# Optimization experiments

Measured on AMD Instinct MI355X. Metric: run time of the kernel, lower is better.

The kernel has to match this reference:

```python
import jax, jax.numpy as jnp
import numpy as np

NUM_EXPERTS = 8
TOP_K = 2
LORA_ALPHA = 2.0
LORA_RANK = 16
D_MODEL = 2048
D_HIDDEN = 5632


def setup_inputs() -> dict:
    key = jax.random.key(0)
    ks = jax.random.split(key, 11)
    B, S, D, H, E, R = 2, 1024, D_MODEL, D_HIDDEN, NUM_EXPERTS, LORA_RANK
    sd = 1.0 / np.sqrt(D)
    sh = 1.0 / np.sqrt(H)
    x = jax.random.normal(ks[0], (B, S, D), jnp.float32)
    gate_w = jax.random.normal(ks[1], (E, D), jnp.float32) * sd   # router Linear(D->E), no bias
    w_up = jax.random.normal(ks[2], (H, D), jnp.float32) * sd     # up_proj.weight
    w_gate = jax.random.normal(ks[3], (H, D), jnp.float32) * sd   # gate_proj.weight
    w_down = jax.random.normal(ks[4], (D, H), jnp.float32) * sh   # down_proj.weight
    up_A = jax.random.normal(ks[5], (E, R, D), jnp.float32) * sd
    up_B = jax.random.normal(ks[6], (E, H, R), jnp.float32) * 0.02
    gate_A = jax.random.normal(ks[7], (E, R, D), jnp.float32) * sd
    gate_B = jax.random.normal(ks[8], (E, H, R), jnp.float32) * 0.02
    down_A = jax.random.normal(ks[9], (E, R, H), jnp.float32) * sh
    down_B = jax.random.normal(ks[10], (E, D, R), jnp.float32) * 0.02
    return {"x": x, "gate_w": gate_w, "w_up": w_up, "w_gate": w_gate,
            "w_down": w_down, "up_A": up_A, "up_B": up_B,
            "gate_A": gate_A, "gate_B": gate_B, "down_A": down_A, "down_B": down_B}


def reference(x, gate_w, w_up, w_gate, w_down, up_A, up_B, gate_A, gate_B, down_A, down_B):
    B, S, D = x.shape
    H = w_up.shape[0]
    # router: logits [B,S,E], top-k over experts (last dim)
    gate_logits = jnp.einsum('bsd,ed->bse', x, gate_w)
    topw, sel = jax.lax.top_k(gate_logits, TOP_K)            # [B,S,k]
    # NOTE: source applies softmax over dim=1 (the SEQUENCE axis) -- reproduced faithfully
    topw = jax.nn.softmax(topw.astype(jnp.float32), axis=1).astype(x.dtype)
    xt = x.reshape(-1, D)                                    # [T, D]
    wf = topw.reshape(-1, TOP_K)                             # [T, k]
    sf = sel.reshape(-1, TOP_K)                              # [T, k]
    # shared base projections computed once for all tokens
    base_up = xt @ w_up.T                                    # [T, H]
    base_gate = xt @ w_gate.T                                # [T, H]
    mixed_h = jnp.zeros((xt.shape[0], H), x.dtype)
    lora_down = jnp.zeros_like(xt)
    # loop over fixed small expert count; low-rank LoRA deltas applied without
    # materializing full merged weights (same math by linearity of matmul)
    for e in range(NUM_EXPERTS):
        c = jnp.sum(jnp.where(sf == e, wf, 0.0), axis=1)     # [T] routing weight (0 if not routed)
        lo_up = LORA_ALPHA * ((xt @ up_A[e].T) @ up_B[e].T)
        lo_gate = LORA_ALPHA * ((xt @ gate_A[e].T) @ gate_B[e].T)
        h_e = jax.nn.silu(base_up + lo_up) * (base_gate + lo_gate)  # [T, H]
        ch = c[:, None] * h_e
        mixed_h = mixed_h + ch
        lora_down = lora_down + LORA_ALPHA * ((ch @ down_A[e].T) @ down_B[e].T)
    out = mixed_h @ w_down.T + lora_down                     # base down GEMM done once on mixed hidden
    return out.reshape(B, S, D)
```

## Files before the change

kernel.cpp:

```cpp
#include <hip/hip_runtime.h>
#include <hip/hip_fp16.h>
#include <cmath>

#define TOKENS 2048
#define DMODEL 2048
#define DHID   5632
#define NEXP   8
#define RANK   16
#define LALPHA 2.0f

typedef __attribute__((ext_vector_type(4))) float f32x4;
typedef __attribute__((ext_vector_type(8))) short s16x8;
typedef __attribute__((ext_vector_type(4))) short s16x4;
typedef __attribute__((ext_vector_type(8))) _Float16 f16x8;

__device__ __forceinline__ short f2bf(float f){
  unsigned u = __float_as_uint(f);
  u += 0x7fffu + ((u >> 16) & 1u);
  return (short)(u >> 16);
}
__device__ __forceinline__ short f2h(float f){
  return (short)__half_as_ushort(__float2half(f));
}

struct Src2 { const short* s0; const short* s1; };

__device__ __forceinline__ Src2 mk_src(const short* g, long ld, int tid){
  Src2 st;
  const int L0 = tid,      r0 = L0>>2, c0 = ((L0&3) - (r0>>1)) & 3;
  const int L1 = 256+tid,  r1 = L1>>2, c1 = ((L1&3) - (r1>>1)) & 3;
  st.s0 = g + (long)r0*ld + c0*8;
  st.s1 = g + (long)r1*ld + c1*8;
  return st;
}
__device__ __forceinline__ void stage2(const Src2& st, int k0, short* t, int tid){
  __builtin_amdgcn_global_load_lds((const __attribute__((address_space(1))) void*)(st.s0 + k0),
                                   (__attribute__((address_space(3))) void*)(t + tid*8), 16, 0, 0);
  __builtin_amdgcn_global_load_lds((const __attribute__((address_space(1))) void*)(st.s1 + k0),
                                   (__attribute__((address_space(3))) void*)(t + (256+tid)*8), 16, 0, 0);
}
__device__ __forceinline__ s16x8 fragb(const short* t, int row, int quad){
  const int p = (quad + (row>>1)) & 3;
  return *(const s16x8*)(t + (row*4 + p)*8);
}
__device__ __forceinline__ f16x8 fragh(const short* t, int row, int quad){
  const int p = (quad + (row>>1)) & 3;
  return *(const f16x8*)(t + (row*4 + p)*8);
}

struct Stage64 { const short* g; short* t; int off[4]; int dof; };

__device__ __forceinline__ Stage64 mk_stage64(const short* g, long ld, short* t, int tid){
  Stage64 st; st.g = g; st.t = t;
  #pragma unroll
  for(int p=0;p<4;p++){
    const int L = p*256 + tid;
    const int r = L>>3, cp = L&7;
    const int c = (cp - (r&7)) & 7;
    st.off[p] = r*(int)ld + c*8;
  }
  st.dof = tid*8;
  return st;
}
__device__ __forceinline__ void do_stage64(const Stage64& st, int k0){
  #pragma unroll
  for(int p=0;p<4;p++)
    __builtin_amdgcn_global_load_lds(
      (const __attribute__((address_space(1))) void*)(st.g + st.off[p] + k0),
      (__attribute__((address_space(3))) void*)(st.t + st.dof + p*2048), 16, 0, 0);
}
__device__ __forceinline__ s16x8 fragb64(const short* t, int row, int ksub, int quad){
  const int c = ksub*4 + quad;
  const int p = (c + (row&7)) & 7;
  return *(const s16x8*)(t + (row*8 + p)*8);
}
__device__ __forceinline__ f16x8 fragh64(const short* t, int row, int ksub, int quad){
  const int c = ksub*4 + quad;
  const int p = (c + (row&7)) & 7;
  return *(const f16x8*)(t + (row*8 + p)*8);
}

__global__ void k_cast(const float* __restrict__ x, const float* __restrict__ w_up,
                       const float* __restrict__ w_gate, const float* __restrict__ w_down,
                       const float* __restrict__ upA, const float* __restrict__ gateA,
                       const float* __restrict__ downA, const float* __restrict__ upB,
                       const float* __restrict__ gateB, const float* __restrict__ downB,
                       short* __restrict__ xb, short* __restrict__ wub, short* __restrict__ wgb,
                       short* __restrict__ wdb, short* __restrict__ daA, short* __restrict__ acat,
                       short* __restrict__ upBcat, short* __restrict__ gateBcat, short* __restrict__ wdbcat){
  const long e0 = 4194304, e1 = 15728640, e2 = 27262976, e3 = 38797312;
  const long e4 = 39518208, e5 = 40042496, e6 = 40763392, e7 = 41484288, e8 = 41746432;
  const long i = ((long)blockIdx.x*256 + threadIdx.x) * 4;
  if(i >= e8) return;
  const float* src; short* dst; long l; int fp16 = 0;
  if(i < e0){ src = x; dst = xb; l = i; }
  else if(i < e1){ src = w_up; dst = wub; l = i - e0; }
  else if(i < e2){ src = w_gate; dst = wgb; l = i - e1; }
  else if(i < e3){ src = w_down; dst = wdb; l = i - e2; }
  else if(i < e4){ src = downA; dst = daA; l = i - e3; }
  else if(i < e5){
    l = i - e4;
    const long c = l>>11;
    const long e = c>>5, pj = (c>>4)&1, r = c&15;
    src = (pj ? gateA : upA) + ((e*RANK + r)<<11) + (l&2047) - l;
    dst = acat;
  }
  else if(i < e6){
    l = i - e5;
    const long h = l>>7, c = l&127, e = c>>4, r = c&15;
    src = upB + ((e*DHID + h)*RANK + r) - l;
    dst = upBcat; fp16 = 1;
  }
  else if(i < e7){
    l = i - e6;
    const long h = l>>7, c = l&127, e = c>>4, r = c&15;
    src = gateB + ((e*DHID + h)*RANK + r) - l;
    dst = gateBcat; fp16 = 1;
  }
  else {
    l = i - e7;
    const long d = l>>7, c = l&127, e = c>>4, r = c&15;
    src = downB + ((e*DMODEL + d)*RANK + r) - l;
    dst = wdbcat; fp16 = 1;
  }
  const float4 v = *(const float4*)(src + l);
  s16x4 o;
  if(fp16){ o[0]=f2h(v.x); o[1]=f2h(v.y); o[2]=f2h(v.z); o[3]=f2h(v.w); }
  else    { o[0]=f2bf(v.x); o[1]=f2bf(v.y); o[2]=f2bf(v.z); o[3]=f2bf(v.w); }
  *(s16x4*)(dst + l) = o;
}

__global__ void k_router(const float* __restrict__ x, const float* __restrict__ gw,
                         int* __restrict__ sel, float* __restrict__ topv){
  const int t = blockIdx.x*4 + (threadIdx.x>>6);
  const int lane = threadIdx.x & 63;
  const float* xr = x + (long)t * DMODEL;
  float acc[NEXP];
  #pragma unroll
  for(int e=0;e<NEXP;e++) acc[e]=0.f;
  #pragma unroll
  for(int it=0; it<8; it++){
    const int d = it*256 + lane*4;
    const float4 xv = *(const float4*)(xr + d);
    #pragma unroll
    for(int e=0;e<NEXP;e++){
      const float4 wv = *(const float4*)(gw + e*DMODEL + d);
      acc[e] += xv.x*wv.x + xv.y*wv.y + xv.z*wv.z + xv.w*wv.w;
    }
  }
  #pragma unroll
  for(int e=0;e<NEXP;e++){
    #pragma unroll
    for(int off=32; off; off>>=1) acc[e] += __shfl_down(acc[e], off, 64);
  }
  if(lane==0){
    int i0=0;
    #pragma unroll
    for(int e=1;e<NEXP;e++) if(acc[e]>acc[i0]) i0=e;
    int i1=-1;
    #pragma unroll
    for(int e=0;e<NEXP;e++){ if(e==i0) continue; if(i1<0 || acc[e]>acc[i1]) i1=e; }
    sel[t*2+0]=i0; sel[t*2+1]=i1;
    topv[t*2+0]=acc[i0]; topv[t*2+1]=acc[i1];
  }
}

__global__ void k_softmax(const float* __restrict__ topv, float* __restrict__ cw){
  const int b = blockIdx.x >> 1, k = blockIdx.x & 1;
  const int base = b*1024;
  __shared__ float red[256];
  float v[4];
  float mx = -1e30f;
  #pragma unroll
  for(int i=0;i<4;i++){
    int s = threadIdx.x + i*256;
    v[i] = topv[(base+s)*2 + k];
    mx = fmaxf(mx, v[i]);
  }
  red[threadIdx.x]=mx; __syncthreads();
  for(int o=128;o;o>>=1){ if(threadIdx.x<o) red[threadIdx.x]=fmaxf(red[threadIdx.x],red[threadIdx.x+o]); __syncthreads(); }
  mx = red[0]; __syncthreads();
  float sum=0.f;
  #pragma unroll
  for(int i=0;i<4;i++){ v[i]=__expf(v[i]-mx); sum+=v[i]; }
  red[threadIdx.x]=sum; __syncthreads();
  for(int o=128;o;o>>=1){ if(threadIdx.x<o) red[threadIdx.x]+=red[threadIdx.x+o]; __syncthreads(); }
  const float inv = 1.f/red[0];
  #pragma unroll
  for(int i=0;i<4;i++){
    int s = threadIdx.x + i*256;
    cw[(base+s)*2+k] = v[i]*inv;
  }
}

__global__ __launch_bounds__(256,2) void k_rank(
    const short* __restrict__ xb, const short* __restrict__ acat, float* __restrict__ Rall){
  __shared__ __align__(16) short At[8192];
  __shared__ __align__(16) short Bt[8192];
  const int c0 = blockIdx.x*128, t0 = blockIdx.y*128;
  const int kbeg = blockIdx.z*256;
  const int tid = threadIdx.x, lane = tid&63, wave = tid>>6;
  const int wm=(wave>>1)*64, wn=(wave&1)*64, fr=lane&15, quad=lane>>4;
  f32x4 acc[4][4];
  #pragma unroll
  for(int i=0;i<4;i++)
    #pragma unroll
    for(int j=0;j<4;j++) acc[i][j]=(f32x4){0.f,0.f,0.f,0.f};
  const Stage64 sA = mk_stage64(xb + (long)t0*DMODEL, DMODEL, At, tid);
  const Stage64 sB = mk_stage64(acat + (long)c0*DMODEL, DMODEL, Bt, tid);
  for(int k0=kbeg; k0<kbeg+256; k0+=64){
    do_stage64(sA, k0); do_stage64(sB, k0);
    __syncthreads();
    #pragma unroll
    for(int s=0;s<2;s++){
      s16x8 af[4];
      #pragma unroll
      for(int i=0;i<4;i++) af[i] = fragb64(At, wm + i*16 + fr, s, quad);
      #pragma unroll
      for(int j=0;j<4;j++){
        const s16x8 bf = fragb64(Bt, wn + j*16 + fr, s, quad);
        #pragma unroll
        for(int i=0;i<4;i++)
          acc[i][j] = __builtin_amdgcn_mfma_f32_16x16x32_bf16(af[i], bf, acc[i][j], 0,0,0);
      }
    }
    __syncthreads();
  }
  #pragma unroll
  for(int i=0;i<4;i++)
    #pragma unroll
    for(int j=0;j<4;j++){
      const int rbase = wm + i*16 + quad*4, col = wn + j*16 + fr;
      #pragma unroll
      for(int reg=0;reg<4;reg++)
        atomicAdd(&Rall[(long)(t0+rbase+reg)*256 + c0 + col], acc[i][j][reg]);
    }
}

__global__ void k_rsel(const float* __restrict__ Rall, const int* __restrict__ sel,
                       short* __restrict__ RselU, short* __restrict__ RselG){
  const int idx = blockIdx.x*256 + threadIdx.x;
  const int c = idx & 127, t = (idx>>7) & (TOKENS-1), k = idx>>18;
  const int e = c>>4, r = c&15;
  const int s = sel[t*2+k];
  const int m = (e==s);
  RselU[idx] = f2h(m ? LALPHA*Rall[(long)t*256 + e*32 + r]      : 0.f);
  RselG[idx] = f2h(m ? LALPHA*Rall[(long)t*256 + e*32 + 16 + r] : 0.f);
}

__global__ __launch_bounds__(256,2) void k_lora(
    const short* __restrict__ RselU, const short* __restrict__ RselG,
    const short* __restrict__ upBcat, const short* __restrict__ gateBcat,
    short* __restrict__ LF){
  __shared__ __align__(16) short At[8192];
  __shared__ __align__(16) short Gt[8192];
  __shared__ __align__(16) short Bt[8192];
  const int h0 = blockIdx.x*128, t0 = blockIdx.y*128;
  const short* Rsel = blockIdx.z ? RselG : RselU;
  const short* Bcat = blockIdx.z ? gateBcat : upBcat;
  const int tid = threadIdx.x, lane = tid&63, wave = tid>>6;
  const int wm=(wave>>1)*64, wn=(wave&1)*64, fr=lane&15, quad=lane>>4;
  f32x4 l0[4][4], l1[4][4];
  #pragma unroll
  for(int i=0;i<4;i++)
    #pragma unroll
    for(int j=0;j<4;j++){ l0[i][j]=(f32x4){0.f,0.f,0.f,0.f}; l1[i][j]=l0[i][j]; }
  const Stage64 sB  = mk_stage64(Bcat + (long)h0*128, 128, Bt, tid);
  const Stage64 sR0 = mk_stage64(Rsel + (long)t0*128, 128, At, tid);
  const Stage64 sR1 = mk_stage64(Rsel + ((long)TOKENS + t0)*128, 128, Gt, tid);
  for(int k0=0; k0<128; k0+=64){
    do_stage64(sB, k0); do_stage64(sR0, k0); do_stage64(sR1, k0);
    __syncthreads();
    #pragma unroll
    for(int s=0;s<2;s++){
      f16x8 a0[4], a1[4];
      #pragma unroll
      for(int i=0;i<4;i++){ a0[i] = fragh64(At, wm + i*16 + fr, s, quad);
                            a1[i] = fragh64(Gt, wm + i*16 + fr, s, quad); }
      #pragma unroll
      for(int j=0;j<4;j++){
        const f16x8 bf = fragh64(Bt, wn + j*16 + fr, s, quad);
        #pragma unroll
        for(int i=0;i<4;i++){
          l0[i][j] = __builtin_amdgcn_mfma_f32_16x16x32_f16(a0[i], bf, l0[i][j], 0,0,0);
          l1[i][j] = __builtin_amdgcn_mfma_f32_16x16x32_f16(a1[i], bf, l1[i][j], 0,0,0);
        }
      }
    }
    __syncthreads();
  }
  short* o = LF + (long)(blockIdx.y*44 + blockIdx.x)*65536 + ((long)blockIdx.z*16*256 + tid)*8;
  #pragma unroll
  for(int i=0;i<4;i++){
    s16x8 p0a, p0b, p1a, p1b;
    #pragma unroll
    for(int r=0;r<4;r++){
      p0a[r]   = f2h(l0[i][0][r]); p0a[4+r] = f2h(l0[i][1][r]);
      p0b[r]   = f2h(l0[i][2][r]); p0b[4+r] = f2h(l0[i][3][r]);
      p1a[r]   = f2h(l1[i][0][r]); p1a[4+r] = f2h(l1[i][1][r]);
      p1b[r]   = f2h(l1[i][2][r]); p1b[4+r] = f2h(l1[i][3][r]);
    }
    *(s16x8*)(o + (i*2+0)*2048)     = p0a;
    *(s16x8*)(o + (i*2+1)*2048)     = p0b;
    *(s16x8*)(o + (8 + i*2+0)*2048) = p1a;
    *(s16x8*)(o + (8 + i*2+1)*2048) = p1b;
  }
}

__global__ __launch_bounds__(256,2) void k_main(
    const short* __restrict__ xb, const short* __restrict__ wub, const short* __restrict__ wgb,
    const short* __restrict__ LF,
    const float* __restrict__ cw, unsigned short* __restrict__ ch, unsigned short* __restrict__ chsum){
  __shared__ __align__(16) short At[3][4096];
  __shared__ __align__(16) short Ut[3][4096];
  __shared__ __align__(16) short Gt[3][4096];
  const int h0 = blockIdx.x*128, t0 = blockIdx.y*128;
  const int tid = threadIdx.x, lane = tid&63, wave = tid>>6;
  const int wm=(wave>>1)*64, wn=(wave&1)*64, fr=lane&15, quad=lane>>4;
  f32x4 au[4][4], ag[4][4];
  #pragma unroll
  for(int i=0;i<4;i++)
    #pragma unroll
    for(int j=0;j<4;j++){ au[i][j]=(f32x4){0.f,0.f,0.f,0.f}; ag[i][j]=au[i][j]; }
  const Src2 sA = mk_src(xb + (long)t0*DMODEL, DMODEL, tid);
  const Src2 sU = mk_src(wub + (long)h0*DMODEL, DMODEL, tid);
  const Src2 sG = mk_src(wgb + (long)h0*DMODEL, DMODEL, tid);

  auto kstep = [&](const short* A, const short* U, const short* G){
    s16x8 af[4];
    #pragma unroll
    for(int i=0;i<4;i++) af[i] = fragb(A, wm + i*16 + fr, quad);
    #pragma unroll
    for(int j=0;j<4;j++){
      const s16x8 bu = fragb(U, wn + j*16 + fr, quad);
      const s16x8 bg = fragb(G, wn + j*16 + fr, quad);
      #pragma unroll
      for(int i=0;i<4;i++){
        au[i][j] = __builtin_amdgcn_mfma_f32_16x16x32_bf16(af[i], bu, au[i][j], 0,0,0);
        ag[i][j] = __builtin_amdgcn_mfma_f32_16x16x32_bf16(af[i], bg, ag[i][j], 0,0,0);
      }
    }
  };

  short *A0=At[0], *A1=At[1], *A2=At[2];
  short *U0=Ut[0], *U1=Ut[1], *U2=Ut[2];
  short *G0=Gt[0], *G1=Gt[1], *G2=Gt[2];
  stage2(sA, 0,  A0, tid); stage2(sU, 0,  U0, tid); stage2(sG, 0,  G0, tid);
  stage2(sA, 32, A1, tid); stage2(sU, 32, U1, tid); stage2(sG, 32, G1, tid);
  for(int s=0; s<62; s++){
    const int k2 = (s+2)*32;
    stage2(sA, k2, A2, tid); stage2(sU, k2, U2, tid); stage2(sG, k2, G2, tid);
    asm volatile("s_waitcnt vmcnt(12)" ::: "memory");
    __builtin_amdgcn_s_barrier();
    __builtin_amdgcn_sched_barrier(0);
    kstep(A0, U0, G0);
    __builtin_amdgcn_sched_barrier(0);
    __builtin_amdgcn_s_barrier();
    short* t;
    t=A0; A0=A1; A1=A2; A2=t;
    t=U0; U0=U1; U1=U2; U2=t;
    t=G0; G0=G1; G1=G2; G2=t;
  }
  asm volatile("s_waitcnt vmcnt(6)" ::: "memory");
  __builtin_amdgcn_s_barrier();
  __builtin_amdgcn_sched_barrier(0);
  kstep(A0, U0, G0);
  __builtin_amdgcn_sched_barrier(0);
  __builtin_amdgcn_s_barrier();
  asm volatile("s_waitcnt vmcnt(0)" ::: "memory");
  __builtin_amdgcn_s_barrier();
  __builtin_amdgcn_sched_barrier(0);
  kstep(A1, U1, G1);

  const short* Lf = LF + (long)(blockIdx.y*44 + blockIdx.x)*65536 + (long)tid*8;
  #pragma unroll
  for(int i=0;i<4;i++){
    f16x8 Uv0[2], Uv1[2], Gv0[2], Gv1[2];
    Uv0[0] = *(const f16x8*)(Lf + (i*2+0)*2048);       Uv0[1] = *(const f16x8*)(Lf + (i*2+1)*2048);
    Uv1[0] = *(const f16x8*)(Lf + (8+i*2+0)*2048);     Uv1[1] = *(const f16x8*)(Lf + (8+i*2+1)*2048);
    Gv0[0] = *(const f16x8*)(Lf + (16+i*2+0)*2048);    Gv0[1] = *(const f16x8*)(Lf + (16+i*2+1)*2048);
    Gv1[0] = *(const f16x8*)(Lf + (24+i*2+0)*2048);    Gv1[1] = *(const f16x8*)(Lf + (24+i*2+1)*2048);
    #pragma unroll
    for(int reg=0;reg<4;reg++){
      const int tl = wm + i*16 + quad*4 + reg;
      const float2 cc = *(const float2*)(cw + (long)(t0+tl)*2);
      const float c0 = cc.x, c1 = cc.y;
      const long row0 = (long)(t0+tl)*DHID + h0;
      const long row1 = ((long)TOKENS + t0+tl)*DHID + h0;
      unsigned short* r0 = ch + row0;
      unsigned short* r1 = ch + row1;
      unsigned short* rs = chsum + row0;
      #pragma unroll
      for(int j=0;j<4;j++){
        const int hl = wn + j*16 + fr;
        const int q = (j&1)*4 + reg, hv = j>>1;
        const float u0 = au[i][j][reg] + (float)Uv0[hv][q];
        const float g0 = ag[i][j][reg] + (float)Gv0[hv][q];
        const float h0v = (u0 / (1.f + __expf(-u0))) * g0;
        const float u1 = au[i][j][reg] + (float)Uv1[hv][q];
        const float g1 = ag[i][j][reg] + (float)Gv1[hv][q];
        const float h1v = (u1 / (1.f + __expf(-u1))) * g1;
        const float v0 = c0*h0v, v1 = c1*h1v;
        r0[hl] = (unsigned short)f2bf(v0);
        r1[hl] = (unsigned short)f2bf(v1);
        rs[hl] = (unsigned short)f2bf(v0+v1);
      }
    }
  }
}

__global__ __launch_bounds__(256,2) void k_rd(
    const unsigned short* __restrict__ ch, const short* __restrict__ daA,
    float* __restrict__ RD){
  __shared__ __align__(16) short At[3][4096];
  __shared__ __align__(16) short Bt[3][4096];
  const int slot = blockIdx.x>>4, ks = blockIdx.x&15;
  const int t0 = blockIdx.y*128;
  const int tid = threadIdx.x, lane = tid&63, wave = tid>>6;
  const int wm=(wave>>1)*64, wn=(wave&1)*64, fr=lane&15, quad=lane>>4;
  f32x4 acc[4][4];
  #pragma unroll
  for(int i=0;i<4;i++)
    #pragma unroll
    for(int j=0;j<4;j++) acc[i][j]=(f32x4){0.f,0.f,0.f,0.f};
  const Src2 sA = mk_src((const short*)ch + ((long)slot*TOKENS + t0)*DHID, DHID, tid);
  const Src2 sB = mk_src(daA, DHID, tid);
  const int kbeg = ks*352;

  auto kstep = [&](const short* A, const short* B){
    s16x8 af[4];
    #pragma unroll
    for(int i=0;i<4;i++) af[i] = fragb(A, wm + i*16 + fr, quad);
    #pragma unroll
    for(int j=0;j<4;j++){
      const s16x8 bf = fragb(B, wn + j*16 + fr, quad);
      #pragma unroll
      for(int i=0;i<4;i++)
        acc[i][j] = __builtin_amdgcn_mfma_f32_16x16x32_bf16(af[i], bf, acc[i][j], 0,0,0);
    }
  };

  short *A0=At[0], *A1=At[1], *A2=At[2];
  short *B0=Bt[0], *B1=Bt[1], *B2=Bt[2];
  stage2(sA, kbeg,    A0, tid); stage2(sB, kbeg,    B0, tid);
  stage2(sA, kbeg+32, A1, tid); stage2(sB, kbeg+32, B1, tid);
  for(int s=0; s<9; s++){
    const int k2 = kbeg + (s+2)*32;
    stage2(sA, k2, A2, tid); stage2(sB, k2, B2, tid);
    asm volatile("s_waitcnt vmcnt(8)" ::: "memory");
    __builtin_amdgcn_s_barrier();
    __builtin_amdgcn_sched_barrier(0);
    kstep(A0, B0);
    __builtin_amdgcn_sched_barrier(0);
    __builtin_amdgcn_s_barrier();
    short* t;
    t=A0; A0=A1; A1=A2; A2=t;
    t=B0; B0=B1; B1=B2; B2=t;
  }
  asm volatile("s_waitcnt vmcnt(4)" ::: "memory");
  __builtin_amdgcn_s_barrier();
  __builtin_amdgcn_sched_barrier(0);
  kstep(A0, B0);
  __builtin_amdgcn_sched_barrier(0);
  __builtin_amdgcn_s_barrier();
  asm volatile("s_waitcnt vmcnt(0)" ::: "memory");
  __builtin_amdgcn_s_barrier();
  __builtin_amdgcn_sched_barrier(0);
  kstep(A1, B1);

  #pragma unroll
  for(int i=0;i<4;i++)
    #pragma unroll
    for(int j=0;j<4;j++){
      const int rbase = wm + i*16 + quad*4, col = wn + j*16 + fr;
      #pragma unroll
      for(int reg=0;reg<4;reg++)
        atomicAdd(&RD[((long)(t0+rbase+reg)*2 + slot)*128 + col], acc[i][j][reg]);
    }
}

__global__ void k_scatter(const float* __restrict__ RD, const int* __restrict__ sel,
                          __half* __restrict__ RDhat){
  const int idx = blockIdx.x*256 + threadIdx.x;
  const int t = idx>>7, c = idx&127, e = c>>4;
  const int s0 = sel[t*2], s1 = sel[t*2+1];
  float v = 0.f;
  if(e == s0) v = LALPHA * RD[((long)t*2+0)*128 + c];
  else if(e == s1) v = LALPHA * RD[((long)t*2+1)*128 + c];
  RDhat[idx] = __float2half(v);
}

__global__ __launch_bounds__(256,2) void k_down(
    const unsigned short* __restrict__ chsum, const short* __restrict__ wdb,
    const short* __restrict__ RDhat, const short* __restrict__ wdbcat,
    float* __restrict__ out){
  __shared__ __align__(16) short At[3][4096];
  __shared__ __align__(16) short Bt[3][4096];
  const int d0 = blockIdx.x*128, t0 = blockIdx.y*128, ks = blockIdx.z;
  const int tid = threadIdx.x, lane = tid&63, wave = tid>>6;
  const int wm=(wave>>1)*64, wn=(wave&1)*64, fr=lane&15, quad=lane>>4;
  f32x4 acc[4][4];
  #pragma unroll
  for(int i=0;i<4;i++)
    #pragma unroll
    for(int j=0;j<4;j++) acc[i][j]=(f32x4){0.f,0.f,0.f,0.f};
  const Src2 sA = mk_src((const short*)chsum + (long)t0*DHID, DHID, tid);
  const Src2 sB = mk_src(wdb + (long)d0*DHID, DHID, tid);
  const int kbeg = ks*2816;

  auto kstep = [&](const short* A, const short* B){
    s16x8 af[4];
    #pragma unroll
    for(int i=0;i<4;i++) af[i] = fragb(A, wm + i*16 + fr, quad);
    #pragma unroll
    for(int j=0;j<4;j++){
      const s16x8 bf = fragb(B, wn + j*16 + fr, quad);
      #pragma unroll
      for(int i=0;i<4;i++)
        acc[i][j] = __builtin_amdgcn_mfma_f32_16x16x32_bf16(af[i], bf, acc[i][j], 0,0,0);
    }
  };

  short *A0=At[0], *A1=At[1], *A2=At[2];
  short *B0=Bt[0], *B1=Bt[1], *B2=Bt[2];
  stage2(sA, kbeg,    A0, tid); stage2(sB, kbeg,    B0, tid);
  stage2(sA, kbeg+32, A1, tid); stage2(sB, kbeg+32, B1, tid);
  for(int s=0; s<86; s++){
    const int k2 = kbeg + (s+2)*32;
    stage2(sA, k2, A2, tid); stage2(sB, k2, B2, tid);
    asm volatile("s_waitcnt vmcnt(8)" ::: "memory");
    __builtin_amdgcn_s_barrier();
    __builtin_amdgcn_sched_barrier(0);
    kstep(A0, B0);
    __builtin_amdgcn_sched_barrier(0);
    __builtin_amdgcn_s_barrier();
    short* t;
    t=A0; A0=A1; A1=A2; A2=t;
    t=B0; B0=B1; B1=B2; B2=t;
  }
  asm volatile("s_waitcnt vmcnt(4)" ::: "memory");
  __builtin_amdgcn_s_barrier();
  __builtin_amdgcn_sched_barrier(0);
  kstep(A0, B0);
  __builtin_amdgcn_sched_barrier(0);
  __builtin_amdgcn_s_barrier();
  asm volatile("s_waitcnt vmcnt(0)" ::: "memory");
  __builtin_amdgcn_s_barrier();
  __builtin_amdgcn_sched_barrier(0);
  kstep(A1, B1);
  __builtin_amdgcn_s_barrier();

  if(ks == 0){
    const Src2 sAh = mk_src(RDhat + (long)t0*128, 128, tid);
    const Src2 sBh = mk_src(wdbcat + (long)d0*128, 128, tid);
    stage2(sAh, 0, At[0], tid); stage2(sBh, 0, Bt[0], tid);
    __syncthreads();
    int cur = 0;
    for(int k0=0; k0<128; k0+=32){
      const int nxt = cur^1;
      if(k0+32 < 128){
        stage2(sAh, k0+32, At[nxt], tid);
        stage2(sBh, k0+32, Bt[nxt], tid);
      }
      __builtin_amdgcn_sched_barrier(0);
      f16x8 af[4];
      #pragma unroll
      for(int i=0;i<4;i++) af[i] = fragh(At[cur], wm + i*16 + fr, quad);
      #pragma unroll
      for(int j=0;j<4;j++){
        const f16x8 bf = fragh(Bt[cur], wn + j*16 + fr, quad);
        #pragma unroll
        for(int i=0;i<4;i++)
          acc[i][j] = __builtin_amdgcn_mfma_f32_16x16x32_f16(af[i], bf, acc[i][j], 0,0,0);
      }
      __syncthreads();
      cur = nxt;
    }
  }
  #pragma unroll
  for(int i=0;i<4;i++)
    #pragma unroll
    for(int j=0;j<4;j++){
      const int rbase = wm + i*16 + quad*4, col = wn + j*16 + fr;
      #pragma unroll
      for(int reg=0;reg<4;reg++)
        atomicAdd(&out[(long)(t0+rbase+reg)*DMODEL + d0 + col], acc[i][j][reg]);
    }
}

extern "C" void kernel_launch(void* const* d_in, const int* in_sizes, int n_in,
                              void* d_out, int out_size, void* d_ws, size_t ws_size,
                              hipStream_t stream){
  (void)in_sizes; (void)n_in; (void)out_size; (void)ws_size;
  const float* x      = (const float*)d_in[0];
  const float* gate_w = (const float*)d_in[1];
  const float* w_up   = (const float*)d_in[2];
  const float* w_gate = (const float*)d_in[3];
  const float* w_down = (const float*)d_in[4];
  const float* up_A   = (const float*)d_in[5];
  const float* up_B   = (const float*)d_in[6];
  const float* gate_A = (const float*)d_in[7];
  const float* gate_B = (const float*)d_in[8];
  const float* down_A = (const float*)d_in[9];
  const float* down_B = (const float*)d_in[10];
  float* out = (float*)d_out;

  char* ws = (char*)d_ws;
  size_t off = 0;
  auto alloc = [&](size_t bytes){ void* p = ws + off; off += (bytes + 255) & ~(size_t)255; return p; };
  short* xb       = (short*)alloc((size_t)TOKENS*DMODEL*2);
  short* wub      = (short*)alloc((size_t)DHID*DMODEL*2);
  short* wgb      = (short*)alloc((size_t)DHID*DMODEL*2);
  short* wdb      = (short*)alloc((size_t)DMODEL*DHID*2);
  short* daA      = (short*)alloc((size_t)128*DHID*2);
  short* acat     = (short*)alloc((size_t)256*DMODEL*2);
  short* upBcat   = (short*)alloc((size_t)DHID*128*2);
  short* gateBcat = (short*)alloc((size_t)DHID*128*2);
  short* wdbcat   = (short*)alloc((size_t)DMODEL*128*2);
  unsigned short* ch    = (unsigned short*)alloc((size_t)2*TOKENS*DHID*2);
  unsigned short* chsum = (unsigned short*)alloc((size_t)TOKENS*DHID*2);
  short* LF     = (short*)alloc((size_t)704*65536*2);
  float* Rall   = (float*)alloc((size_t)TOKENS*256*4);
  short* RselU  = (short*)alloc((size_t)2*TOKENS*128*2);
  short* RselG  = (short*)alloc((size_t)2*TOKENS*128*2);
  float* RD     = (float*)alloc((size_t)TOKENS*2*128*4);
  __half* RDhat = (__half*)alloc((size_t)TOKENS*128*2);
  int*   sel    = (int*)alloc((size_t)TOKENS*2*4);
  float* topv   = (float*)alloc((size_t)TOKENS*2*4);
  float* cw     = (float*)alloc((size_t)TOKENS*2*4);

  (void)hipMemsetAsync(RD, 0, (size_t)TOKENS*2*128*4, stream);
  (void)hipMemsetAsync(Rall, 0, (size_t)TOKENS*256*4, stream);
  (void)hipMemsetAsync(out, 0, (size_t)TOKENS*DMODEL*4, stream);
  k_cast<<<40768, 256, 0, stream>>>(x, w_up, w_gate, w_down, up_A, gate_A, down_A,
                                    up_B, gate_B, down_B,
                                    xb, wub, wgb, wdb, daA, acat, upBcat, gateBcat, wdbcat);
  k_router<<<512, 256, 0, stream>>>(x, gate_w, sel, topv);
  k_softmax<<<4, 256, 0, stream>>>(topv, cw);
  k_rank<<<dim3(2,16,8), 256, 0, stream>>>(xb, acat, Rall);
  k_rsel<<<2048, 256, 0, stream>>>(Rall, sel, RselU, RselG);
  k_lora<<<dim3(44,16,2), 256, 0, stream>>>(RselU, RselG, upBcat, gateBcat, LF);
  k_main<<<dim3(44,16), 256, 0, stream>>>(xb, wub, wgb, LF, cw, ch, chsum);
  k_rd<<<dim3(32,16), 256, 0, stream>>>(ch, daA, RD);
  k_scatter<<<1024, 256, 0, stream>>>(RD, sel, RDhat);
  k_down<<<dim3(16,16,2), 256, 0, stream>>>(chsum, wdb, (const short*)RDhat, wdbcat, out);
}
```

Measured before the change: 537.9 us.

## Restructure fused up/gate GEMM to 256x128 tiles with 512 threads and phased prefetch

Rewrites k_main to use 512-thread blocks computing 256-token by 128-hidden tiles with BK=64, double-buffered LDS, and swizzled global_load_lds prefetch split across four MFMA phases with s_setprio. The larger M tile doubles reuse of the weight tiles and halves the number of blocks along tokens, cutting global traffic for the weight operand. It also interleaves the loads with the compute phases to hide latency. The cost is more barriers per iteration, higher LDS use (about 128KB), and an epilogue that has to remap the LF layout to the new wave arrangement.

```diff
diff --git a/kernel.cpp b/kernel.cpp
--- a/kernel.cpp
+++ b/kernel.cpp
@@ -79,6 +79,10 @@
   const int p = (c + (row&7)) & 7;
   return *(const f16x8*)(t + (row*8 + p)*8);
 }
+
+#define GLL(SRC, DST) __builtin_amdgcn_global_load_lds( \
+    (const __attribute__((address_space(1))) void*)(SRC), \
+    (__attribute__((address_space(3))) void*)(DST), 16, 0, 0)
 
 __global__ void k_cast(const float* __restrict__ x, const float* __restrict__ w_up,
                        const float* __restrict__ w_gate, const float* __restrict__ w_down,
@@ -307,103 +311,145 @@
   }
 }
 
-__global__ __launch_bounds__(256,2) void k_main(
+#define MFMA_P(P) do{ \
+  __builtin_amdgcn_s_setprio(1); \
+  _Pragma("unroll") for(int ks=0;ks<2;ks++){ \
+    _Pragma("unroll") for(int ii=0;ii<2;ii++){ \
+      _Pragma("unroll") for(int j=0;j<2;j++){ \
+        aU[2*(P)+ii][j] = __builtin_amdgcn_mfma_f32_16x16x32_bf16(a[ii][ks], bu[j][ks], aU[2*(P)+ii][j],0,0,0); \
+        aG[2*(P)+ii][j] = __builtin_amdgcn_mfma_f32_16x16x32_bf16(a[ii][ks], bg[j][ks], aG[2*(P)+ii][j],0,0,0); \
+      }}} \
+  __builtin_amdgcn_s_setprio(0); }while(0)
+
+#define RDA(P) do{ \
+  _Pragma("unroll") for(int ii=0;ii<2;ii++){ \
+    _Pragma("unroll") for(int ks=0;ks<2;ks++){ \
+      a[ii][ks] = fragb64(Ac, rbaseA + (2*(P)+ii)*16 + fr, ks, quad); \
+    }}}while(0)
+
+__global__ __launch_bounds__(512,2) void k_main(
     const short* __restrict__ xb, const short* __restrict__ wub, const short* __restrict__ wgb,
-    const short* __restrict__ LF,
-    const float* __restrict__ cw, unsigned short* __restrict__ ch, unsigned short* __restrict__ chsum){
-  __shared__ __align__(16) short At[3][4096];
-  __shared__ __align__(16) short Ut[3][4096];
-  __shared__ __align__(16) short Gt[3][4096];
-  const int h0 = blockIdx.x*128, t0 = blockIdx.y*128;
-  const int tid = threadIdx.x, lane = tid&63, wave = tid>>6;
-  const int wm=(wave>>1)*64, wn=(wave&1)*64, fr=lane&15, quad=lane>>4;
-  f32x4 au[4][4], ag[4][4];
-  #pragma unroll
-  for(int i=0;i<4;i++)
-    #pragma unroll
-    for(int j=0;j<4;j++){ au[i][j]=(f32x4){0.f,0.f,0.f,0.f}; ag[i][j]=au[i][j]; }
-  const Src2 sA = mk_src(xb + (long)t0*DMODEL, DMODEL, tid);
-  const Src2 sU = mk_src(wub + (long)h0*DMODEL, DMODEL, tid);
-  const Src2 sG = mk_src(wgb + (long)h0*DMODEL, DMODEL, tid);
-
-  auto kstep = [&](const short* A, const short* U, const short* G){
-    s16x8 af[4];
-    #pragma unroll
-    for(int i=0;i<4;i++) af[i] = fragb(A, wm + i*16 + fr, quad);
-    #pragma unroll
-    for(int j=0;j<4;j++){
-      const s16x8 bu = fragb(U, wn + j*16 + fr, quad);
-      const s16x8 bg = fragb(G, wn + j*16 + fr, quad);
-      #pragma unroll
-      for(int i=0;i<4;i++){
-        au[i][j] = __builtin_amdgcn_mfma_f32_16x16x32_bf16(af[i], bu, au[i][j], 0,0,0);
-        ag[i][j] = __builtin_amdgcn_mfma_f32_16x16x32_bf16(af[i], bg, ag[i][j], 0,0,0);
+    const short* __restrict__ LF, const float* __restrict__ cw,
+    unsigned short* __restrict__ ch, unsigned short* __restrict__ chsum){
+  __shared__ __align__(16) short AL[2][16384];
+  __shared__ __align__(16) short UL[2][8192];
+  __shared__ __align__(16) short GL[2][8192];
+  const int bh = blockIdx.x, bt = blockIdx.y;
+  const int tid = threadIdx.x;
+  const int w = tid>>6, lane = tid&63, fr = lane&15, quad = lane>>4;
+  const int wq = w>>2, wh = w&3;
+  const int rbaseA = wq*128;
+  const int rbaseB = wh*32;
+  const short* gA = xb  + (long)bt*256*DMODEL;
+  const short* gU = wub + (long)bh*128*DMODEL;
+  const short* gG = wgb + (long)bh*128*DMODEL;
+  int offA[4], offB[2];
+  #pragma unroll
+  for(int k=0;k<4;k++){ const int L=k*512+tid, r=L>>3, p=L&7, c=(p-(r&7))&7; offA[k]=r*DMODEL+c*8; }
+  #pragma unroll
+  for(int k=0;k<2;k++){ const int L=k*512+tid, r=L>>3, p=L&7, c=(p-(r&7))&7; offB[k]=r*DMODEL+c*8; }
+
+  f32x4 aU[8][2], aG[8][2];
+  #pragma unroll
+  for(int i=0;i<8;i++)
+    #pragma unroll
+    for(int j=0;j<2;j++){ aU[i][j]=(f32x4){0.f,0.f,0.f,0.f}; aG[i][j]=aU[i][j]; }
+
+  short *Ac=AL[0], *An=AL[1], *Uc=UL[0], *Un=UL[1], *Gc=GL[0], *Gn=GL[1];
+  #pragma unroll
+  for(int k=0;k<4;k++) GLL(gA+offA[k], Ac+(k*512+tid)*8);
+  #pragma unroll
+  for(int k=0;k<2;k++){ GLL(gU+offB[k], Uc+(k*512+tid)*8); GLL(gG+offB[k], Gc+(k*512+tid)*8); }
+
+  auto iter = [&](int k0n, bool pf) __attribute__((always_inline)) {
+    if(pf){ GLL(gA+offA[0]+k0n, An+(0*512+tid)*8); GLL(gA+offA[1]+k0n, An+(1*512+tid)*8);
+            asm volatile("s_waitcnt vmcnt(2)" ::: "memory"); }
+    else  { asm volatile("s_waitcnt vmcnt(0)" ::: "memory"); }
+    __builtin_amdgcn_sched_barrier(0);
+    __builtin_amdgcn_s_barrier();
+    __builtin_amdgcn_sched_barrier(0);
+    s16x8 bu[2][2], bg[2][2];
+    #pragma unroll
+    for(int j=0;j<2;j++)
+      #pragma unroll
+      for(int ks=0;ks<2;ks++){
+        bu[j][ks] = fragb64(Uc, rbaseB + j*16 + fr, ks, quad);
+        bg[j][ks] = fragb64(Gc, rbaseB + j*16 + fr, ks, quad);
       }
-    }
+    s16x8 a[2][2];
+    RDA(0);
+    MFMA_P(0);
+    __builtin_amdgcn_sched_barrier(0);
+    __builtin_amdgcn_s_barrier();
+    if(pf){ GLL(gA+offA[2]+k0n, An+(2*512+tid)*8); GLL(gA+offA[3]+k0n, An+(3*512+tid)*8); }
+    RDA(1);
+    __builtin_amdgcn_sched_barrier(0);
+    __builtin_amdgcn_s_barrier();
+    __builtin_amdgcn_sched_barrier(0);
+    MFMA_P(1);
+    __builtin_amdgcn_sched_barrier(0);
+    __builtin_amdgcn_s_barrier();
+    if(pf){ GLL(gU+offB[0]+k0n, Un+(0*512+tid)*8); GLL(gU+offB[1]+k0n, Un+(1*512+tid)*8); }
+    RDA(2);
+    __builtin_amdgcn_sched_barrier(0);
+    __builtin_amdgcn_s_barrier();
+    __builtin_amdgcn_sched_barrier(0);
+    MFMA_P(2);
+    __builtin_amdgcn_sched_barrier(0);
+    __builtin_amdgcn_s_barrier();
+    if(pf){ GLL(gG+offB[0]+k0n, Gn+(0*512+tid)*8); GLL(gG+offB[1]+k0n, Gn+(1*512+tid)*8); }
+    RDA(3);
+    __builtin_amdgcn_sched_barrier(0);
+    __builtin_amdgcn_s_barrier();
+    __builtin_amdgcn_sched_barrier(0);
+    MFMA_P(3);
+    __builtin_amdgcn_sched_barrier(0);
+    __builtin_amdgcn_s_barrier();
   };
 
-  short *A0=At[0], *A1=At[1], *A2=At[2];
-  short *U0=Ut[0], *U1=Ut[1], *U2=Ut[2];
-  short *G0=Gt[0], *G1=Gt[1], *G2=Gt[2];
-  stage2(sA, 0,  A0, tid); stage2(sU, 0,  U0, tid); stage2(sG, 0,  G0, tid);
-  stage2(sA, 32, A1, tid); stage2(sU, 32, U1, tid); stage2(sG, 32, G1, tid);
-  for(int s=0; s<62; s++){
-    const int k2 = (s+2)*32;
-    stage2(sA, k2, A2, tid); stage2(sU, k2, U2, tid); stage2(sG, k2, G2, tid);
-    asm volatile("s_waitcnt vmcnt(12)" ::: "memory");
-    __builtin_amdgcn_s_barrier();
-    __builtin_amdgcn_sched_barrier(0);
-    kstep(A0, U0, G0);
-    __builtin_amdgcn_sched_barrier(0);
-    __builtin_amdgcn_s_barrier();
-    short* t;
-    t=A0; A0=A1; A1=A2; A2=t;
-    t=U0; U0=U1; U1=U2; U2=t;
-    t=G0; G0=G1; G1=G2; G2=t;
-  }
-  asm volatile("s_waitcnt vmcnt(6)" ::: "memory");
-  __builtin_amdgcn_s_barrier();
-  __builtin_amdgcn_sched_barrier(0);
-  kstep(A0, U0, G0);
-  __builtin_amdgcn_sched_barrier(0);
-  __builtin_amdgcn_s_barrier();
-  asm volatile("s_waitcnt vmcnt(0)" ::: "memory");
-  __builtin_amdgcn_s_barrier();
-  __builtin_amdgcn_sched_barrier(0);
-  kstep(A1, U1, G1);
-
-  const short* Lf = LF + (long)(blockIdx.y*44 + blockIdx.x)*65536 + (long)tid*8;
-  #pragma unroll
-  for(int i=0;i<4;i++){
-    f16x8 Uv0[2], Uv1[2], Gv0[2], Gv1[2];
-    Uv0[0] = *(const f16x8*)(Lf + (i*2+0)*2048);       Uv0[1] = *(const f16x8*)(Lf + (i*2+1)*2048);
-    Uv1[0] = *(const f16x8*)(Lf + (8+i*2+0)*2048);     Uv1[1] = *(const f16x8*)(Lf + (8+i*2+1)*2048);
-    Gv0[0] = *(const f16x8*)(Lf + (16+i*2+0)*2048);    Gv0[1] = *(const f16x8*)(Lf + (16+i*2+1)*2048);
-    Gv1[0] = *(const f16x8*)(Lf + (24+i*2+0)*2048);    Gv1[1] = *(const f16x8*)(Lf + (24+i*2+1)*2048);
+  #pragma unroll 1
+  for(int t=0; t<31; t++){
+    iter((t+1)*64, true);
+    short* tmp;
+    tmp=Ac; Ac=An; An=tmp;
+    tmp=Uc; Uc=Un; Un=tmp;
+    tmp=Gc; Gc=Gn; Gn=tmp;
+  }
+  iter(0, false);
+
+  const long LFB = (long)((bt*2 + wq)*44 + bh)*65536;
+  const int h0c = bh*128 + wh*32;
+  #pragma unroll
+  for(int i=0;i<8;i++){
+    const int wp = (i>>2)*2 + (wh>>1);
+    const int tidp = wp*64 + quad*16 + fr;
+    const short* base = LF + LFB + (long)tidp*8;
+    const int qb = (i&3)*2 + (wh&1);
+    const f16x8 Uv0 = *(const f16x8*)(base + (long)(qb)*2048);
+    const f16x8 Uv1 = *(const f16x8*)(base + (long)(8+qb)*2048);
+    const f16x8 Gv0 = *(const f16x8*)(base + (long)(16+qb)*2048);
+    const f16x8 Gv1 = *(const f16x8*)(base + (long)(24+qb)*2048);
     #pragma unroll
     for(int reg=0;reg<4;reg++){
-      const int tl = wm + i*16 + quad*4 + reg;
-      const float2 cc = *(const float2*)(cw + (long)(t0+tl)*2);
-      const float c0 = cc.x, c1 = cc.y;
-      const long row0 = (long)(t0+tl)*DHID + h0;
-      const long row1 = ((long)TOKENS + t0+tl)*DHID + h0;
-      unsigned short* r0 = ch + row0;
-      unsigned short* r1 = ch + row1;
-      unsigned short* rs = chsum + row0;
-      #pragma unroll
-      for(int j=0;j<4;j++){
-        const int hl = wn + j*16 + fr;
-        const int q = (j&1)*4 + reg, hv = j>>1;
-        const float u0 = au[i][j][reg] + (float)Uv0[hv][q];
-        const float g0 = ag[i][j][reg] + (float)Gv0[hv][q];
+      const int t = bt*256 + wq*128 + i*16 + quad*4 + reg;
+      const float2 cc = *(const float2*)(cw + (long)t*2);
+      unsigned short* r0 = ch + (long)t*DHID;
+      unsigned short* r1 = ch + ((long)TOKENS + t)*DHID;
+      unsigned short* rs = chsum + (long)t*DHID;
+      #pragma unroll
+      for(int j=0;j<2;j++){
+        const int h = h0c + j*16 + fr;
+        const int idx = j*4 + reg;
+        const float u0 = aU[i][j][reg] + (float)Uv0[idx];
+        const float g0 = aG[i][j][reg] + (float)Gv0[idx];
         const float h0v = (u0 / (1.f + __expf(-u0))) * g0;
-        const float u1 = au[i][j][reg] + (float)Uv1[hv][q];
-        const float g1 = ag[i][j][reg] + (float)Gv1[hv][q];
+        const float u1 = aU[i][j][reg] + (float)Uv1[idx];
+        const float g1 = aG[i][j][reg] + (float)Gv1[idx];
         const float h1v = (u1 / (1.f + __expf(-u1))) * g1;
-        const float v0 = c0*h0v, v1 = c1*h1v;
-        r0[hl] = (unsigned short)f2bf(v0);
-        r1[hl] = (unsigned short)f2bf(v1);
-        rs[hl] = (unsigned short)f2bf(v0+v1);
+        const float v0 = cc.x*h0v, v1 = cc.y*h1v;
+        r0[h] = (unsigned short)f2bf(v0);
+        r1[h] = (unsigned short)f2bf(v1);
+        rs[h] = (unsigned short)f2bf(v0+v1);
       }
     }
   }
@@ -640,7 +686,7 @@
   k_rank<<<dim3(2,16,8), 256, 0, stream>>>(xb, acat, Rall);
   k_rsel<<<2048, 256, 0, stream>>>(Rall, sel, RselU, RselG);
   k_lora<<<dim3(44,16,2), 256, 0, stream>>>(RselU, RselG, upBcat, gateBcat, LF);
-  k_main<<<dim3(44,16), 256, 0, stream>>>(xb, wub, wgb, LF, cw, ch, chsum);
+  k_main<<<dim3(44,8), 512, 0, stream>>>(xb, wub, wgb, LF, cw, ch, chsum);
   k_rd<<<dim3(32,16), 256, 0, stream>>>(ch, daA, RD);
   k_scatter<<<1024, 256, 0, stream>>>(RD, sel, RDhat);
   k_down<<<dim3(16,16,2), 256, 0, stream>>>(chsum, wdb, (const short*)RDhat, wdbcat, out);
```

New measurement: 533.8 us. About the same (-0.8%).

## Replace triple-buffered GEMM pipeline with double buffering and stage routing weights in LDS

Applied to the files above, without the earlier changes.

The main up/gate GEMM loop drops the three-stage LDS ring with explicit vmcnt waits and uses a simpler double-buffered loop with __syncthreads per k-step. LDS use falls from three to two buffers per operand, which may help occupancy. The per-token routing weights are loaded once into shared memory instead of read from global memory in the epilogue. Prefetch depth shrinks and each iteration waits on all outstanding loads, so global load latency may be exposed more than before.

```diff
diff --git a/kernel.cpp b/kernel.cpp
--- a/kernel.cpp
+++ b/kernel.cpp
@@ -311,12 +311,14 @@
     const short* __restrict__ xb, const short* __restrict__ wub, const short* __restrict__ wgb,
     const short* __restrict__ LF,
     const float* __restrict__ cw, unsigned short* __restrict__ ch, unsigned short* __restrict__ chsum){
-  __shared__ __align__(16) short At[3][4096];
-  __shared__ __align__(16) short Ut[3][4096];
-  __shared__ __align__(16) short Gt[3][4096];
+  __shared__ __align__(16) short At[2][4096];
+  __shared__ __align__(16) short Ut[2][4096];
+  __shared__ __align__(16) short Gt[2][4096];
+  __shared__ float cwv[128][2];
   const int h0 = blockIdx.x*128, t0 = blockIdx.y*128;
   const int tid = threadIdx.x, lane = tid&63, wave = tid>>6;
   const int wm=(wave>>1)*64, wn=(wave&1)*64, fr=lane&15, quad=lane>>4;
+  { const int tl = tid>>1, k = tid&1; cwv[tl][k] = cw[(t0+tl)*2 + k]; }
   f32x4 au[4][4], ag[4][4];
   #pragma unroll
   for(int i=0;i<4;i++)
@@ -325,53 +327,33 @@
   const Src2 sA = mk_src(xb + (long)t0*DMODEL, DMODEL, tid);
   const Src2 sU = mk_src(wub + (long)h0*DMODEL, DMODEL, tid);
   const Src2 sG = mk_src(wgb + (long)h0*DMODEL, DMODEL, tid);
-
-  auto kstep = [&](const short* A, const short* U, const short* G){
+  stage2(sA, 0, At[0], tid); stage2(sU, 0, Ut[0], tid); stage2(sG, 0, Gt[0], tid);
+  __syncthreads();
+  int cur = 0;
+  for(int k0=0; k0<DMODEL; k0+=32){
+    const int nxt = cur^1;
+    if(k0+32 < DMODEL){
+      stage2(sA, k0+32, At[nxt], tid);
+      stage2(sU, k0+32, Ut[nxt], tid);
+      stage2(sG, k0+32, Gt[nxt], tid);
+    }
+    __builtin_amdgcn_sched_barrier(0);
     s16x8 af[4];
     #pragma unroll
-    for(int i=0;i<4;i++) af[i] = fragb(A, wm + i*16 + fr, quad);
+    for(int i=0;i<4;i++) af[i] = fragb(At[cur], wm + i*16 + fr, quad);
     #pragma unroll
     for(int j=0;j<4;j++){
-      const s16x8 bu = fragb(U, wn + j*16 + fr, quad);
-      const s16x8 bg = fragb(G, wn + j*16 + fr, quad);
+      const s16x8 bu = fragb(Ut[cur], wn + j*16 + fr, quad);
+      const s16x8 bg = fragb(Gt[cur], wn + j*16 + fr, quad);
       #pragma unroll
       for(int i=0;i<4;i++){
         au[i][j] = __builtin_amdgcn_mfma_f32_16x16x32_bf16(af[i], bu, au[i][j], 0,0,0);
         ag[i][j] = __builtin_amdgcn_mfma_f32_16x16x32_bf16(af[i], bg, ag[i][j], 0,0,0);
       }
     }
-  };
-
-  short *A0=At[0], *A1=At[1], *A2=At[2];
-  short *U0=Ut[0], *U1=Ut[1], *U2=Ut[2];
-  short *G0=Gt[0], *G1=Gt[1], *G2=Gt[2];
-  stage2(sA, 0,  A0, tid); stage2(sU, 0,  U0, tid); stage2(sG, 0,  G0, tid);
-  stage2(sA, 32, A1, tid); stage2(sU, 32, U1, tid); stage2(sG, 32, G1, tid);
-  for(int s=0; s<62; s++){
-    const int k2 = (s+2)*32;
-    stage2(sA, k2, A2, tid); stage2(sU, k2, U2, tid); stage2(sG, k2, G2, tid);
-    asm volatile("s_waitcnt vmcnt(12)" ::: "memory");
-    __builtin_amdgcn_s_barrier();
-    __builtin_amdgcn_sched_barrier(0);
-    kstep(A0, U0, G0);
-    __builtin_amdgcn_sched_barrier(0);
-    __builtin_amdgcn_s_barrier();
-    short* t;
-    t=A0; A0=A1; A1=A2; A2=t;
-    t=U0; U0=U1; U1=U2; U2=t;
-    t=G0; G0=G1; G1=G2; G2=t;
-  }
-  asm volatile("s_waitcnt vmcnt(6)" ::: "memory");
-  __builtin_amdgcn_s_barrier();
-  __builtin_amdgcn_sched_barrier(0);
-  kstep(A0, U0, G0);
-  __builtin_amdgcn_sched_barrier(0);
-  __builtin_amdgcn_s_barrier();
-  asm volatile("s_waitcnt vmcnt(0)" ::: "memory");
-  __builtin_amdgcn_s_barrier();
-  __builtin_amdgcn_sched_barrier(0);
-  kstep(A1, U1, G1);
-
+    __syncthreads();
+    cur = nxt;
+  }
   const short* Lf = LF + (long)(blockIdx.y*44 + blockIdx.x)*65536 + (long)tid*8;
   #pragma unroll
   for(int i=0;i<4;i++){
@@ -383,8 +365,7 @@
     #pragma unroll
     for(int reg=0;reg<4;reg++){
       const int tl = wm + i*16 + quad*4 + reg;
-      const float2 cc = *(const float2*)(cw + (long)(t0+tl)*2);
-      const float c0 = cc.x, c1 = cc.y;
+      const float c0 = cwv[tl][0], c1 = cwv[tl][1];
       const long row0 = (long)(t0+tl)*DHID + h0;
       const long row1 = ((long)TOKENS + t0+tl)*DHID + h0;
       unsigned short* r0 = ch + row0;
```

After: 539.2 us. About the same (+0.2%).
